# Kernel tuning notes

Measured on AMD Instinct MI355X. Metric: run time of the kernel, lower is better.

The kernel has to match this reference:

```python
import jax, jax.numpy as jnp
import numpy as np

NUM_GROUPS = 8
EPS = 1e-6


def group_norm(x, scale, bias):
    # x: [b, c, h, w]
    b, c, h, w = x.shape
    g = NUM_GROUPS
    xg = x.reshape(b, g, c // g, h, w)
    mean = jnp.mean(xg, axis=(2, 3, 4), keepdims=True)
    var = jnp.var(xg, axis=(2, 3, 4), keepdims=True)
    xg = (xg - mean) * jax.lax.rsqrt(var + EPS)
    xn = xg.reshape(b, c, h, w)
    return xn * scale[None, :, None, None] + bias[None, :, None, None]


def conv1x1(x, w, b):
    # 1x1 conv == channel-mixing matmul. x: [b,c,h,w], w: [co,ci], b: [co]
    return jnp.einsum('oc,bchw->bohw', w, x) + b[None, :, None, None]


def setup_inputs() -> dict:
    key = jax.random.key(0)
    ks = jax.random.split(key, 11)
    b, c, h, w = 8, 256, 64, 64
    s = 1.0 / np.sqrt(c)
    return {
        'x': jax.random.normal(ks[0], (b, c, h, w), dtype=jnp.float32),
        'gn_scale': jnp.ones((c,), dtype=jnp.float32),
        'gn_bias': jnp.zeros((c,), dtype=jnp.float32),
        'wq': jax.random.normal(ks[1], (c, c), dtype=jnp.float32) * s,
        'bq': jax.random.normal(ks[2], (c,), dtype=jnp.float32) * 0.01,
        'wk': jax.random.normal(ks[3], (c, c), dtype=jnp.float32) * s,
        'bk': jax.random.normal(ks[4], (c,), dtype=jnp.float32) * 0.01,
        'wv': jax.random.normal(ks[5], (c, c), dtype=jnp.float32) * s,
        'bv': jax.random.normal(ks[6], (c,), dtype=jnp.float32) * 0.01,
        'wo': jax.random.normal(ks[7], (c, c), dtype=jnp.float32) * s,
        'bo': jax.random.normal(ks[8], (c,), dtype=jnp.float32) * 0.01,
    }


def reference(x, gn_scale, gn_bias, wq, bq, wk, bk, wv, bv, wo, bo):
    b, c, h, w = x.shape
    hn = group_norm(x, gn_scale, gn_bias)
    q = conv1x1(hn, wq, bq).reshape(b, c, h * w)  # [b,c,n]
    k = conv1x1(hn, wk, bk).reshape(b, c, h * w)
    v = conv1x1(hn, wv, bv).reshape(b, c, h * w)
    scale = jnp.asarray(c, x.dtype) ** -0.5
    attn = jnp.einsum('bci,bcj->bij', q, k) * scale  # [b,n,n]
    attn = jax.nn.softmax(attn, axis=2)
    out = jnp.einsum('bcj,bij->bci', v, attn)  # [b,c,n]
    out = out.reshape(b, c, h, w)
    return x + conv1x1(out, wo, bo)
```

## Files before the change

kernel.cpp:

```cpp
#include <hip/hip_runtime.h>

typedef __bf16 bf16;
typedef __bf16 bf16x8 __attribute__((ext_vector_type(8)));
typedef float  f32x4  __attribute__((ext_vector_type(4)));

#define NSP 4096
#define NCH 256
#define NB  8

static __device__ __forceinline__ void glds16(const bf16* g, bf16* l) {
  __builtin_amdgcn_global_load_lds(
      (const __attribute__((address_space(1))) unsigned int*)g,
      (__attribute__((address_space(3))) unsigned int*)l, 16, 0, 0);
}

__global__ __launch_bounds__(256) void k_wconv(
    const float* __restrict__ wq, const float* __restrict__ wk,
    const float* __restrict__ wv, const float* __restrict__ wo,
    bf16* __restrict__ wbf) {
  int g = blockIdx.x * 256 + threadIdx.x;
  int m = g >> 16, idx = g & 65535;
  const float* src = (m == 0) ? wq : (m == 1) ? wk : (m == 2) ? wv : wo;
  float sc = (m == 0) ? 0.0625f : 1.0f;
  wbf[g] = (bf16)(src[idx] * sc);
}

__global__ __launch_bounds__(256) void k_gnstats1(const float* __restrict__ x,
                                                  float2* __restrict__ part) {
  int blk = blockIdx.x;
  int bg = blk >> 3, seg = blk & 7;
  const float4* p = (const float4*)(x + (size_t)bg * 131072 + seg * 16384);
  float s = 0.f, s2 = 0.f;
  for (int i = threadIdx.x; i < 4096; i += 256) {
    float4 v = p[i];
    s  += v.x + v.y + v.z + v.w;
    s2 += v.x*v.x + v.y*v.y + v.z*v.z + v.w*v.w;
  }
  for (int off = 1; off < 64; off <<= 1) {
    s  += __shfl_xor(s, off);
    s2 += __shfl_xor(s2, off);
  }
  __shared__ float a1[4], a2[4];
  int w = threadIdx.x >> 6, lane = threadIdx.x & 63;
  if (lane == 0) { a1[w] = s; a2[w] = s2; }
  __syncthreads();
  if (threadIdx.x == 0)
    part[blk] = make_float2(a1[0]+a1[1]+a1[2]+a1[3], a2[0]+a2[1]+a2[2]+a2[3]);
}

__global__ __launch_bounds__(64) void k_gnstats2(const float2* __restrict__ part,
                                                 float* __restrict__ stats) {
  int bg = threadIdx.x;
  float s = 0.f, s2 = 0.f;
  #pragma unroll
  for (int k = 0; k < 8; ++k) {
    float2 v = part[bg * 8 + k];
    s += v.x; s2 += v.y;
  }
  float mean = s * (1.f / 131072.f);
  float var  = s2 * (1.f / 131072.f) - mean * mean;
  stats[bg * 2]     = mean;
  stats[bg * 2 + 1] = rsqrtf(var + 1e-6f);
}

__global__ __launch_bounds__(256) void k_gnapply(const float* __restrict__ x,
    const float* __restrict__ stats, const float* __restrict__ gsc,
    const float* __restrict__ gbi, bf16* __restrict__ hnT) {
  __shared__ float T[64][65];
  int blk = blockIdx.x;
  int b = blk >> 8, ct = (blk >> 6) & 3, it = blk & 63;
  int tid = threadIdx.x;
  #pragma unroll 4
  for (int p = 0; p < 16; ++p) {
    int cc = p * 4 + (tid >> 6), ii = tid & 63;
    int c = ct * 64 + cc;
    float mean = stats[(b * 8 + (c >> 5)) * 2];
    float rstd = stats[(b * 8 + (c >> 5)) * 2 + 1];
    float v = x[((size_t)b * NCH + c) * NSP + it * 64 + ii];
    T[cc][ii] = (v - mean) * rstd * gsc[c] + gbi[c];
  }
  __syncthreads();
  #pragma unroll 4
  for (int p = 0; p < 16; ++p) {
    int ii = p * 4 + (tid >> 6), cc = tid & 63;
    hnT[((size_t)b * NSP + it * 64 + ii) * NCH + ct * 64 + cc] = (bf16)T[cc][ii];
  }
}

__global__ __launch_bounds__(256, 4) void k_qkv(const bf16* __restrict__ hnT,
    const bf16* __restrict__ wbf, const float* __restrict__ bq,
    const float* __restrict__ bk, const float* __restrict__ bv,
    bf16* __restrict__ qT, bf16* __restrict__ kS, bf16* __restrict__ vS) {
  const int pass = blockIdx.x >> 9;
  const int rem  = blockIdx.x & 511;
  const int b  = rem >> 6;
  const int i0 = (rem & 63) * 64;
  const int tid = threadIdx.x, w = tid >> 6, lane = tid & 63;
  const int li = lane & 15, qd = lane >> 4;
  const bf16* W = wbf + (size_t)pass * 65536;

  if (pass == 2) {
    f32x4 acc[16];
    #pragma unroll
    for (int t = 0; t < 16; ++t) acc[t] = (f32x4){0.f, 0.f, 0.f, 0.f};
    for (int kc = 0; kc < 8; ++kc) {
      bf16x8 hb = *(const bf16x8*)(hnT + ((size_t)b * NSP + i0 + w * 16 + li) * NCH + kc * 32 + qd * 8);
      #pragma unroll
      for (int ct = 0; ct < 16; ++ct) {
        bf16x8 wf = *(const bf16x8*)(W + (size_t)(ct * 16 + li) * NCH + kc * 32 + qd * 8);
        acc[ct] = __builtin_amdgcn_mfma_f32_16x16x32_bf16(hb, wf, acc[ct], 0, 0, 0);
      }
    }
    int jloc = w * 16 + qd * 4;
    size_t base = (size_t)b * 1048576 + (size_t)((i0 + jloc) >> 5) * 8192;
    int j32 = jloc & 31;
    int g  = (j32 >> 2) & 3;
    int hi = j32 >> 4;
    #pragma unroll
    for (int ct = 0; ct < 16; ++ct) {
      int co = ct * 16 + li;
      float bb = bv[co];
      int pg = g ^ ((co >> 1) & 3);
      union { bf16 h[4]; uint2 u; } pk;
      #pragma unroll
      for (int r = 0; r < 4; ++r) pk.h[r] = (bf16)(acc[ct][r] + bb);
      *(uint2*)(vS + base + (size_t)(co * 4 + pg) * 8 + hi * 4) = pk.u;
    }
    return;
  }

  f32x4 acc[16];
  #pragma unroll
  for (int t = 0; t < 16; ++t) acc[t] = (f32x4){0.f, 0.f, 0.f, 0.f};
  for (int kc = 0; kc < 8; ++kc) {
    bf16x8 hb[4];
    #pragma unroll
    for (int nt = 0; nt < 4; ++nt)
      hb[nt] = *(const bf16x8*)(hnT + ((size_t)b * NSP + i0 + nt * 16 + li) * NCH + kc * 32 + qd * 8);
    #pragma unroll
    for (int mt = 0; mt < 4; ++mt) {
      bf16x8 wf = *(const bf16x8*)(W + (size_t)(w * 64 + mt * 16 + li) * NCH + kc * 32 + qd * 8);
      #pragma unroll
      for (int nt = 0; nt < 4; ++nt)
        acc[mt * 4 + nt] = __builtin_amdgcn_mfma_f32_16x16x32_bf16(wf, hb[nt], acc[mt * 4 + nt], 0, 0, 0);
    }
  }

  if (pass == 0) {
    bf16* out = qT + ((size_t)b * NSP + i0) * NCH;
    #pragma unroll
    for (int mt = 0; mt < 4; ++mt) {
      float bb[4];
      #pragma unroll
      for (int r = 0; r < 4; ++r) bb[r] = bq[w * 64 + mt * 16 + qd * 4 + r] * 0.0625f;
      #pragma unroll
      for (int nt = 0; nt < 4; ++nt) {
        union { bf16 h[4]; uint2 u; } pk;
        #pragma unroll
        for (int r = 0; r < 4; ++r) pk.h[r] = (bf16)(acc[mt * 4 + nt][r] + bb[r]);
        *(uint2*)(out + (size_t)(nt * 16 + li) * NCH + w * 64 + mt * 16 + qd * 4) = pk.u;
      }
    }
  } else {
    #pragma unroll
    for (int mt = 0; mt < 4; ++mt) {
      float bb[4];
      #pragma unroll
      for (int r = 0; r < 4; ++r) bb[r] = bk[w * 64 + mt * 16 + qd * 4 + r];
      int cb = w * 8 + mt * 2 + (qd >> 1);
      #pragma unroll
      for (int nt = 0; nt < 4; ++nt) {
        int jloc = nt * 16 + li;
        size_t base = (size_t)b * 1048576 + (size_t)((i0 + jloc) >> 5) * 8192;
        int r32 = jloc & 31;
        union { bf16 h[4]; uint2 u; } pk;
        #pragma unroll
        for (int r = 0; r < 4; ++r) pk.h[r] = (bf16)(acc[mt * 4 + nt][r] + bb[r]);
        *(uint2*)(kS + base + r32 * 256 + (cb ^ (r32 & 7)) * 8 + (qd & 1) * 4) = pk.u;
      }
    }
  }
}

__global__ __launch_bounds__(256, 2) void k_attn(const bf16* __restrict__ qT,
    const bf16* __restrict__ kS, const bf16* __restrict__ vS,
    bf16* __restrict__ Op0, bf16* __restrict__ Op1, float* __restrict__ Lp) {
  __shared__ bf16 Kb[2][8192];
  __shared__ bf16 Vt[8192];

  const int bjs = blockIdx.x & 15;
  const int itb = blockIdx.x >> 4;
  const int b = bjs >> 1, js = bjs & 1;
  const int i0 = itb * 128;
  const int tid = threadIdx.x, w = tid >> 6, lane = tid & 63;
  const int li = lane & 15, qd = lane >> 4;

  const bf16* kS_b = kS + (size_t)b * 1048576 + (size_t)js * 524288;
  const bf16* vS_b = vS + (size_t)b * 1048576 + (size_t)js * 524288;

  bf16x8 qf[2][8];
  #pragma unroll
  for (int it = 0; it < 2; ++it) {
    const bf16* qp = qT + ((size_t)b * NSP + i0 + w * 32 + it * 16 + li) * NCH + qd * 8;
    #pragma unroll
    for (int kc = 0; kc < 8; ++kc) qf[it][kc] = *(const bf16x8*)(qp + kc * 32);
  }

  f32x4 Oa[2][16];
  #pragma unroll
  for (int it = 0; it < 2; ++it)
    #pragma unroll
    for (int t = 0; t < 16; ++t) Oa[it][t] = (f32x4){0.f, 0.f, 0.f, 0.f};
  float lacc[2] = {0.f, 0.f};

  int4 Rv[4];
  #pragma unroll
  for (int p = 0; p < 4; ++p)
    glds16(kS_b + (size_t)(w * 256 + p * 64 + lane) * 8, &Kb[0][(w * 256 + p * 64) * 8]);
  #pragma unroll
  for (int p = 0; p < 4; ++p)
    Rv[p] = *(const int4*)(vS_b + (size_t)(p * 256 + tid) * 8);

  const int pgv = qd ^ ((li >> 1) & 3);

  for (int jc = 0; jc < 64; ++jc) {
    const int cur = jc & 1;
    __syncthreads();
    #pragma unroll
    for (int p = 0; p < 4; ++p)
      *(int4*)(&Vt[(size_t)(p * 256 + tid) * 8]) = Rv[p];
    __syncthreads();

    {
      const int jn = (jc < 63) ? jc + 1 : 63;
      const bf16* kt = kS_b + (size_t)jn * 8192;
      const bf16* vt = vS_b + (size_t)jn * 8192;
      #pragma unroll
      for (int p = 0; p < 4; ++p)
        glds16(kt + (size_t)(w * 256 + p * 64 + lane) * 8, &Kb[cur ^ 1][(w * 256 + p * 64) * 8]);
      #pragma unroll
      for (int p = 0; p < 4; ++p)
        Rv[p] = *(const int4*)(vt + (size_t)(p * 256 + tid) * 8);
    }

    const bf16* Kc = Kb[cur];
    f32x4 S[2][2];
    S[0][0] = (f32x4){0.f,0.f,0.f,0.f}; S[0][1] = (f32x4){0.f,0.f,0.f,0.f};
    S[1][0] = (f32x4){0.f,0.f,0.f,0.f}; S[1][1] = (f32x4){0.f,0.f,0.f,0.f};
    #pragma unroll
    for (int jt = 0; jt < 2; ++jt) {
      #pragma unroll
      for (int kc = 0; kc < 8; ++kc) {
        int pb = (kc * 4 + qd) ^ (li & 7);
        bf16x8 kf = *(const bf16x8*)(Kc + (jt * 16 + li) * 256 + pb * 8);
        S[0][jt] = __builtin_amdgcn_mfma_f32_16x16x32_bf16(kf, qf[0][kc], S[0][jt], 0, 0, 0);
        S[1][jt] = __builtin_amdgcn_mfma_f32_16x16x32_bf16(kf, qf[1][kc], S[1][jt], 0, 0, 0);
      }
    }

    bf16x8 pf[2];
    #pragma unroll
    for (int it = 0; it < 2; ++it)
      #pragma unroll
      for (int jt = 0; jt < 2; ++jt)
        #pragma unroll
        for (int r = 0; r < 4; ++r) {
          float e = __expf(S[it][jt][r] - 8.f);
          lacc[it] += e;
          pf[it][jt * 4 + r] = (bf16)e;
        }

    #pragma unroll
    for (int ct = 0; ct < 16; ++ct) {
      bf16x8 vf = *(const bf16x8*)(&Vt[(size_t)(ct * 16 + li) * 32 + pgv * 8]);
      Oa[0][ct] = __builtin_amdgcn_mfma_f32_16x16x32_bf16(vf, pf[0], Oa[0][ct], 0, 0, 0);
      Oa[1][ct] = __builtin_amdgcn_mfma_f32_16x16x32_bf16(vf, pf[1], Oa[1][ct], 0, 0, 0);
    }
  }

  float lfull[2], linv[2];
  #pragma unroll
  for (int it = 0; it < 2; ++it) {
    float v = lacc[it];
    v += __shfl_xor(v, 16);
    v += __shfl_xor(v, 32);
    lfull[it] = v;
    linv[it] = 1.f / v;
  }

  bf16* Op = js ? Op1 : Op0;
  #pragma unroll
  for (int it = 0; it < 2; ++it) {
    bf16* op = Op + ((size_t)b * NSP + i0 + w * 32 + it * 16 + li) * NCH;
    #pragma unroll
    for (int ct = 0; ct < 16; ++ct) {
      union { bf16 h[4]; uint2 u; } pk;
      pk.h[0] = (bf16)(Oa[it][ct][0] * linv[it]);
      pk.h[1] = (bf16)(Oa[it][ct][1] * linv[it]);
      pk.h[2] = (bf16)(Oa[it][ct][2] * linv[it]);
      pk.h[3] = (bf16)(Oa[it][ct][3] * linv[it]);
      *(uint2*)(op + ct * 16 + qd * 4) = pk.u;
    }
  }
  if (qd == 0) {
    float* lp = Lp + js * 32768 + b * 4096 + i0 + w * 32;
    #pragma unroll
    for (int it = 0; it < 2; ++it) lp[it * 16 + li] = lfull[it];
  }
}

__global__ __launch_bounds__(256, 4) void k_out(const bf16* __restrict__ Op0,
    const bf16* __restrict__ Op1, const float* __restrict__ Lp,
    const bf16* __restrict__ wo, const float* __restrict__ bo,
    const float* __restrict__ x, float* __restrict__ out) {
  const int b  = blockIdx.x >> 7;
  const int i0 = ((blockIdx.x >> 1) & 63) * 64;
  const int ch = blockIdx.x & 1;
  const int tid = threadIdx.x, w = tid >> 6, lane = tid & 63;
  const int li = lane & 15, qd = lane >> 4;
  const int cb0 = ch * 128 + w * 32;

  float w0[4], w1[4];
  #pragma unroll
  for (int nt = 0; nt < 4; ++nt) {
    int i = b * 4096 + i0 + nt * 16 + li;
    float l0 = Lp[i], l1 = Lp[32768 + i];
    float inv = 1.f / (l0 + l1);
    w0[nt] = l0 * inv; w1[nt] = l1 * inv;
  }

  f32x4 acc[8];
  #pragma unroll
  for (int t = 0; t < 8; ++t) acc[t] = (f32x4){0.f, 0.f, 0.f, 0.f};
  for (int kc = 0; kc < 8; ++kc) {
    bf16x8 ab[4];
    #pragma unroll
    for (int nt = 0; nt < 4; ++nt) {
      size_t off = ((size_t)b * NSP + i0 + nt * 16 + li) * NCH + kc * 32 + qd * 8;
      bf16x8 a0 = *(const bf16x8*)(Op0 + off);
      bf16x8 a1 = *(const bf16x8*)(Op1 + off);
      #pragma unroll
      for (int e = 0; e < 8; ++e)
        ab[nt][e] = (bf16)(w0[nt] * (float)a0[e] + w1[nt] * (float)a1[e]);
    }
    #pragma unroll
    for (int mt = 0; mt < 2; ++mt) {
      bf16x8 wf = *(const bf16x8*)(wo + (size_t)(cb0 + mt * 16 + li) * NCH + kc * 32 + qd * 8);
      #pragma unroll
      for (int nt = 0; nt < 4; ++nt)
        acc[mt * 4 + nt] = __builtin_amdgcn_mfma_f32_16x16x32_bf16(wf, ab[nt], acc[mt * 4 + nt], 0, 0, 0);
    }
  }
  #pragma unroll
  for (int mt = 0; mt < 2; ++mt) {
    #pragma unroll
    for (int r = 0; r < 4; ++r) {
      int co = cb0 + mt * 16 + qd * 4 + r;
      float bb = bo[co];
      #pragma unroll
      for (int nt = 0; nt < 4; ++nt) {
        size_t idx = ((size_t)b * NCH + co) * NSP + i0 + nt * 16 + li;
        out[idx] = acc[mt * 4 + nt][r] + bb + x[idx];
      }
    }
  }
}

extern "C" void kernel_launch(void* const* d_in, const int* in_sizes, int n_in,
                              void* d_out, int out_size, void* d_ws, size_t ws_size,
                              hipStream_t stream) {
  (void)in_sizes; (void)n_in; (void)out_size; (void)ws_size;
  const float* x   = (const float*)d_in[0];
  const float* gsc = (const float*)d_in[1];
  const float* gbi = (const float*)d_in[2];
  const float* wq  = (const float*)d_in[3];
  const float* bq  = (const float*)d_in[4];
  const float* wk  = (const float*)d_in[5];
  const float* bk  = (const float*)d_in[6];
  const float* wv  = (const float*)d_in[7];
  const float* bv  = (const float*)d_in[8];
  const float* wo  = (const float*)d_in[9];
  const float* bo  = (const float*)d_in[10];

  char* ws = (char*)d_ws;
  const size_t MB16 = 16777216u;
  bf16*   wbf   = (bf16*)(ws);
  float*  stats = (float*)(ws + 524288);
  float2* part  = (float2*)(ws + 528384);
  float*  Lp    = (float*)(ws + 655360);
  bf16*   hnT   = (bf16*)(ws + (1u << 20));
  bf16*   qT    = (bf16*)(ws + (1u << 20) + 1 * MB16);
  bf16*   kS    = (bf16*)(ws + (1u << 20) + 2 * MB16);
  bf16*   vS    = (bf16*)(ws + (1u << 20) + 3 * MB16);
  bf16*   Op1   = (bf16*)(ws + (1u << 20) + 4 * MB16);
  bf16*   Op0   = hnT;
  float*  out   = (float*)d_out;

  k_wconv   <<<1024, 256, 0, stream>>>(wq, wk, wv, wo, wbf);
  k_gnstats1<<< 512, 256, 0, stream>>>(x, part);
  k_gnstats2<<<   1,  64, 0, stream>>>(part, stats);
  k_gnapply <<<2048, 256, 0, stream>>>(x, stats, gsc, gbi, hnT);
  k_qkv     <<<1536, 256, 0, stream>>>(hnT, wbf, bq, bk, bv, qT, kS, vS);
  k_attn    <<< 512, 256, 0, stream>>>(qT, kS, vS, Op0, Op1, Lp);
  k_out     <<<1024, 256, 0, stream>>>(Op0, Op1, Lp, wbf + 3ull * 65536, bo, x, out);
}
```

Baseline: 456.4 us.

## Merge prep kernels, fuse QKV passes via LDS, stream V directly in attention

Merges the weight-conversion and group-norm statistics kernels into a single launch. The QKV kernel now stages each hidden tile in swizzled LDS once and computes Q, K and V from it in one block, instead of using three separate block sets that each reread hnT. The attention kernel drops the V LDS staging and its extra barrier, changes the vS layout so each lane can load its V fragments straight from global memory interleaved with the QK MFMAs, and stops issuing the redundant final K prefetch. In exchange the attention loop takes on global-load latency and higher register pressure, and the QKV grid shrinks to 512 blocks, which reduces parallelism.

```diff
diff --git a/kernel.cpp b/kernel.cpp
--- a/kernel.cpp
+++ b/kernel.cpp
@@ -14,38 +14,37 @@
       (__attribute__((address_space(3))) unsigned int*)l, 16, 0, 0);
 }
 
-__global__ __launch_bounds__(256) void k_wconv(
+__global__ __launch_bounds__(256) void k_prep(const float* __restrict__ x,
     const float* __restrict__ wq, const float* __restrict__ wk,
     const float* __restrict__ wv, const float* __restrict__ wo,
-    bf16* __restrict__ wbf) {
-  int g = blockIdx.x * 256 + threadIdx.x;
-  int m = g >> 16, idx = g & 65535;
-  const float* src = (m == 0) ? wq : (m == 1) ? wk : (m == 2) ? wv : wo;
-  float sc = (m == 0) ? 0.0625f : 1.0f;
-  wbf[g] = (bf16)(src[idx] * sc);
-}
-
-__global__ __launch_bounds__(256) void k_gnstats1(const float* __restrict__ x,
-                                                  float2* __restrict__ part) {
-  int blk = blockIdx.x;
-  int bg = blk >> 3, seg = blk & 7;
-  const float4* p = (const float4*)(x + (size_t)bg * 131072 + seg * 16384);
-  float s = 0.f, s2 = 0.f;
-  for (int i = threadIdx.x; i < 4096; i += 256) {
-    float4 v = p[i];
-    s  += v.x + v.y + v.z + v.w;
-    s2 += v.x*v.x + v.y*v.y + v.z*v.z + v.w*v.w;
-  }
-  for (int off = 1; off < 64; off <<= 1) {
-    s  += __shfl_xor(s, off);
-    s2 += __shfl_xor(s2, off);
-  }
-  __shared__ float a1[4], a2[4];
-  int w = threadIdx.x >> 6, lane = threadIdx.x & 63;
-  if (lane == 0) { a1[w] = s; a2[w] = s2; }
-  __syncthreads();
-  if (threadIdx.x == 0)
-    part[blk] = make_float2(a1[0]+a1[1]+a1[2]+a1[3], a2[0]+a2[1]+a2[2]+a2[3]);
+    bf16* __restrict__ wbf, float2* __restrict__ part) {
+  if (blockIdx.x < 512) {
+    int blk = blockIdx.x;
+    int bg = blk >> 3, seg = blk & 7;
+    const float4* p = (const float4*)(x + (size_t)bg * 131072 + seg * 16384);
+    float s = 0.f, s2 = 0.f;
+    for (int i = threadIdx.x; i < 4096; i += 256) {
+      float4 v = p[i];
+      s  += v.x + v.y + v.z + v.w;
+      s2 += v.x*v.x + v.y*v.y + v.z*v.z + v.w*v.w;
+    }
+    for (int off = 1; off < 64; off <<= 1) {
+      s  += __shfl_xor(s, off);
+      s2 += __shfl_xor(s2, off);
+    }
+    __shared__ float a1[4], a2[4];
+    int w = threadIdx.x >> 6, lane = threadIdx.x & 63;
+    if (lane == 0) { a1[w] = s; a2[w] = s2; }
+    __syncthreads();
+    if (threadIdx.x == 0)
+      part[blk] = make_float2(a1[0]+a1[1]+a1[2]+a1[3], a2[0]+a2[1]+a2[2]+a2[3]);
+  } else {
+    int g = (blockIdx.x - 512) * 256 + threadIdx.x;
+    int m = g >> 16, idx = g & 65535;
+    const float* src = (m == 0) ? wq : (m == 1) ? wk : (m == 2) ? wv : wo;
+    float sc = (m == 0) ? 0.0625f : 1.0f;
+    wbf[g] = (bf16)(src[idx] * sc);
+  }
 }
 
 __global__ __launch_bounds__(64) void k_gnstats2(const float2* __restrict__ part,
@@ -91,20 +90,83 @@
     const bf16* __restrict__ wbf, const float* __restrict__ bq,
     const float* __restrict__ bk, const float* __restrict__ bv,
     bf16* __restrict__ qT, bf16* __restrict__ kS, bf16* __restrict__ vS) {
-  const int pass = blockIdx.x >> 9;
-  const int rem  = blockIdx.x & 511;
-  const int b  = rem >> 6;
-  const int i0 = (rem & 63) * 64;
+  __shared__ bf16 hnS[64 * 256];
+  const int b  = blockIdx.x >> 6;
+  const int i0 = (blockIdx.x & 63) * 64;
   const int tid = threadIdx.x, w = tid >> 6, lane = tid & 63;
   const int li = lane & 15, qd = lane >> 4;
-  const bf16* W = wbf + (size_t)pass * 65536;
-
-  if (pass == 2) {
+
+  #pragma unroll
+  for (int p = 0; p < 8; ++p) {
+    int idx = p * 256 + tid;
+    int i = idx >> 5, g = idx & 31;
+    bf16x8 v = *(const bf16x8*)(hnT + ((size_t)b * NSP + i0 + i) * NCH + g * 8);
+    *(bf16x8*)(&hnS[i * 256 + (g ^ (i & 7)) * 8]) = v;
+  }
+  __syncthreads();
+
+  #pragma unroll 1
+  for (int pass = 0; pass < 2; ++pass) {
+    const bf16* W = wbf + (size_t)pass * 65536;
     f32x4 acc[16];
     #pragma unroll
     for (int t = 0; t < 16; ++t) acc[t] = (f32x4){0.f, 0.f, 0.f, 0.f};
     for (int kc = 0; kc < 8; ++kc) {
-      bf16x8 hb = *(const bf16x8*)(hnT + ((size_t)b * NSP + i0 + w * 16 + li) * NCH + kc * 32 + qd * 8);
+      bf16x8 hb[4];
+      #pragma unroll
+      for (int nt = 0; nt < 4; ++nt)
+        hb[nt] = *(const bf16x8*)(&hnS[(nt * 16 + li) * 256 + ((kc * 4 + qd) ^ (li & 7)) * 8]);
+      #pragma unroll
+      for (int mt = 0; mt < 4; ++mt) {
+        bf16x8 wf = *(const bf16x8*)(W + (size_t)(w * 64 + mt * 16 + li) * NCH + kc * 32 + qd * 8);
+        #pragma unroll
+        for (int nt = 0; nt < 4; ++nt)
+          acc[mt * 4 + nt] = __builtin_amdgcn_mfma_f32_16x16x32_bf16(wf, hb[nt], acc[mt * 4 + nt], 0, 0, 0);
+      }
+    }
+    if (pass == 0) {
+      bf16* out = qT + ((size_t)b * NSP + i0) * NCH;
+      #pragma unroll
+      for (int mt = 0; mt < 4; ++mt) {
+        float bb[4];
+        #pragma unroll
+        for (int r = 0; r < 4; ++r) bb[r] = bq[w * 64 + mt * 16 + qd * 4 + r] * 0.0625f;
+        #pragma unroll
+        for (int nt = 0; nt < 4; ++nt) {
+          union { bf16 h[4]; uint2 u; } pk;
+          #pragma unroll
+          for (int r = 0; r < 4; ++r) pk.h[r] = (bf16)(acc[mt * 4 + nt][r] + bb[r]);
+          *(uint2*)(out + (size_t)(nt * 16 + li) * NCH + w * 64 + mt * 16 + qd * 4) = pk.u;
+        }
+      }
+    } else {
+      #pragma unroll
+      for (int mt = 0; mt < 4; ++mt) {
+        float bb[4];
+        #pragma unroll
+        for (int r = 0; r < 4; ++r) bb[r] = bk[w * 64 + mt * 16 + qd * 4 + r];
+        int cb = w * 8 + mt * 2 + (qd >> 1);
+        #pragma unroll
+        for (int nt = 0; nt < 4; ++nt) {
+          int jloc = nt * 16 + li;
+          size_t base = (size_t)b * 1048576 + (size_t)((i0 + jloc) >> 5) * 8192;
+          int r32 = jloc & 31;
+          union { bf16 h[4]; uint2 u; } pk;
+          #pragma unroll
+          for (int r = 0; r < 4; ++r) pk.h[r] = (bf16)(acc[mt * 4 + nt][r] + bb[r]);
+          *(uint2*)(kS + base + r32 * 256 + (cb ^ (r32 & 7)) * 8 + (qd & 1) * 4) = pk.u;
+        }
+      }
+    }
+  }
+
+  {
+    const bf16* W = wbf + 2ull * 65536;
+    f32x4 acc[16];
+    #pragma unroll
+    for (int t = 0; t < 16; ++t) acc[t] = (f32x4){0.f, 0.f, 0.f, 0.f};
+    for (int kc = 0; kc < 8; ++kc) {
+      bf16x8 hb = *(const bf16x8*)(&hnS[(w * 16 + li) * 256 + ((kc * 4 + qd) ^ (li & 7)) * 8]);
       #pragma unroll
       for (int ct = 0; ct < 16; ++ct) {
         bf16x8 wf = *(const bf16x8*)(W + (size_t)(ct * 16 + li) * NCH + kc * 32 + qd * 8);
@@ -113,71 +175,14 @@
     }
     int jloc = w * 16 + qd * 4;
     size_t base = (size_t)b * 1048576 + (size_t)((i0 + jloc) >> 5) * 8192;
-    int j32 = jloc & 31;
-    int g  = (j32 >> 2) & 3;
-    int hi = j32 >> 4;
     #pragma unroll
     for (int ct = 0; ct < 16; ++ct) {
       int co = ct * 16 + li;
       float bb = bv[co];
-      int pg = g ^ ((co >> 1) & 3);
       union { bf16 h[4]; uint2 u; } pk;
       #pragma unroll
       for (int r = 0; r < 4; ++r) pk.h[r] = (bf16)(acc[ct][r] + bb);
-      *(uint2*)(vS + base + (size_t)(co * 4 + pg) * 8 + hi * 4) = pk.u;
-    }
-    return;
-  }
-
-  f32x4 acc[16];
-  #pragma unroll
-  for (int t = 0; t < 16; ++t) acc[t] = (f32x4){0.f, 0.f, 0.f, 0.f};
-  for (int kc = 0; kc < 8; ++kc) {
-    bf16x8 hb[4];
-    #pragma unroll
-    for (int nt = 0; nt < 4; ++nt)
-      hb[nt] = *(const bf16x8*)(hnT + ((size_t)b * NSP + i0 + nt * 16 + li) * NCH + kc * 32 + qd * 8);
-    #pragma unroll
-    for (int mt = 0; mt < 4; ++mt) {
-      bf16x8 wf = *(const bf16x8*)(W + (size_t)(w * 64 + mt * 16 + li) * NCH + kc * 32 + qd * 8);
-      #pragma unroll
-      for (int nt = 0; nt < 4; ++nt)
-        acc[mt * 4 + nt] = __builtin_amdgcn_mfma_f32_16x16x32_bf16(wf, hb[nt], acc[mt * 4 + nt], 0, 0, 0);
-    }
-  }
-
-  if (pass == 0) {
-    bf16* out = qT + ((size_t)b * NSP + i0) * NCH;
-    #pragma unroll
-    for (int mt = 0; mt < 4; ++mt) {
-      float bb[4];
-      #pragma unroll
-      for (int r = 0; r < 4; ++r) bb[r] = bq[w * 64 + mt * 16 + qd * 4 + r] * 0.0625f;
-      #pragma unroll
-      for (int nt = 0; nt < 4; ++nt) {
-        union { bf16 h[4]; uint2 u; } pk;
-        #pragma unroll
-        for (int r = 0; r < 4; ++r) pk.h[r] = (bf16)(acc[mt * 4 + nt][r] + bb[r]);
-        *(uint2*)(out + (size_t)(nt * 16 + li) * NCH + w * 64 + mt * 16 + qd * 4) = pk.u;
-      }
-    }
-  } else {
-    #pragma unroll
-    for (int mt = 0; mt < 4; ++mt) {
-      float bb[4];
-      #pragma unroll
-      for (int r = 0; r < 4; ++r) bb[r] = bk[w * 64 + mt * 16 + qd * 4 + r];
-      int cb = w * 8 + mt * 2 + (qd >> 1);
-      #pragma unroll
-      for (int nt = 0; nt < 4; ++nt) {
-        int jloc = nt * 16 + li;
-        size_t base = (size_t)b * 1048576 + (size_t)((i0 + jloc) >> 5) * 8192;
-        int r32 = jloc & 31;
-        union { bf16 h[4]; uint2 u; } pk;
-        #pragma unroll
-        for (int r = 0; r < 4; ++r) pk.h[r] = (bf16)(acc[mt * 4 + nt][r] + bb[r]);
-        *(uint2*)(kS + base + r32 * 256 + (cb ^ (r32 & 7)) * 8 + (qd & 1) * 4) = pk.u;
-      }
+      *(uint2*)(vS + base + (size_t)co * 32 + qd * 8 + (w & 1) * 4) = pk.u;
     }
   }
 }
@@ -186,7 +191,6 @@
     const bf16* __restrict__ kS, const bf16* __restrict__ vS,
     bf16* __restrict__ Op0, bf16* __restrict__ Op1, float* __restrict__ Lp) {
   __shared__ bf16 Kb[2][8192];
-  __shared__ bf16 Vt[8192];
 
   const int bjs = blockIdx.x & 15;
   const int itb = blockIdx.x >> 4;
@@ -196,7 +200,8 @@
   const int li = lane & 15, qd = lane >> 4;
 
   const bf16* kS_b = kS + (size_t)b * 1048576 + (size_t)js * 524288;
-  const bf16* vS_b = vS + (size_t)b * 1048576 + (size_t)js * 524288;
+  const bf16* vS_b = vS + (size_t)b * 1048576 + (size_t)js * 524288
+                   + li * 32 + qd * 8;
 
   bf16x8 qf[2][8];
   #pragma unroll
@@ -213,50 +218,47 @@
     for (int t = 0; t < 16; ++t) Oa[it][t] = (f32x4){0.f, 0.f, 0.f, 0.f};
   float lacc[2] = {0.f, 0.f};
 
-  int4 Rv[4];
   #pragma unroll
   for (int p = 0; p < 4; ++p)
     glds16(kS_b + (size_t)(w * 256 + p * 64 + lane) * 8, &Kb[0][(w * 256 + p * 64) * 8]);
-  #pragma unroll
-  for (int p = 0; p < 4; ++p)
-    Rv[p] = *(const int4*)(vS_b + (size_t)(p * 256 + tid) * 8);
-
-  const int pgv = qd ^ ((li >> 1) & 3);
 
   for (int jc = 0; jc < 64; ++jc) {
     const int cur = jc & 1;
     __syncthreads();
-    #pragma unroll
-    for (int p = 0; p < 4; ++p)
-      *(int4*)(&Vt[(size_t)(p * 256 + tid) * 8]) = Rv[p];
-    __syncthreads();
-
-    {
-      const int jn = (jc < 63) ? jc + 1 : 63;
-      const bf16* kt = kS_b + (size_t)jn * 8192;
-      const bf16* vt = vS_b + (size_t)jn * 8192;
+    if (jc < 63) {
+      const bf16* kt = kS_b + (size_t)(jc + 1) * 8192;
       #pragma unroll
       for (int p = 0; p < 4; ++p)
         glds16(kt + (size_t)(w * 256 + p * 64 + lane) * 8, &Kb[cur ^ 1][(w * 256 + p * 64) * 8]);
-      #pragma unroll
-      for (int p = 0; p < 4; ++p)
-        Rv[p] = *(const int4*)(vt + (size_t)(p * 256 + tid) * 8);
-    }
+    }
+    const bf16* vt = vS_b + (size_t)jc * 8192;
+
+    bf16x8 vf0[4], vf1[4], vf2[4], vf3[4];
+    #pragma unroll
+    for (int u = 0; u < 4; ++u) vf0[u] = *(const bf16x8*)(vt + u * 512);
 
     const bf16* Kc = Kb[cur];
     f32x4 S[2][2];
     S[0][0] = (f32x4){0.f,0.f,0.f,0.f}; S[0][1] = (f32x4){0.f,0.f,0.f,0.f};
     S[1][0] = (f32x4){0.f,0.f,0.f,0.f}; S[1][1] = (f32x4){0.f,0.f,0.f,0.f};
     #pragma unroll
-    for (int jt = 0; jt < 2; ++jt) {
-      #pragma unroll
-      for (int kc = 0; kc < 8; ++kc) {
-        int pb = (kc * 4 + qd) ^ (li & 7);
-        bf16x8 kf = *(const bf16x8*)(Kc + (jt * 16 + li) * 256 + pb * 8);
-        S[0][jt] = __builtin_amdgcn_mfma_f32_16x16x32_bf16(kf, qf[0][kc], S[0][jt], 0, 0, 0);
-        S[1][jt] = __builtin_amdgcn_mfma_f32_16x16x32_bf16(kf, qf[1][kc], S[1][jt], 0, 0, 0);
-      }
-    }
+    for (int kc = 0; kc < 8; ++kc) {
+      int pb = (kc * 4 + qd) ^ (li & 7);
+      bf16x8 kf = *(const bf16x8*)(Kc + li * 256 + pb * 8);
+      S[0][0] = __builtin_amdgcn_mfma_f32_16x16x32_bf16(kf, qf[0][kc], S[0][0], 0, 0, 0);
+      S[1][0] = __builtin_amdgcn_mfma_f32_16x16x32_bf16(kf, qf[1][kc], S[1][0], 0, 0, 0);
+    }
+    #pragma unroll
+    for (int u = 0; u < 4; ++u) vf1[u] = *(const bf16x8*)(vt + (4 + u) * 512);
+    #pragma unroll
+    for (int kc = 0; kc < 8; ++kc) {
+      int pb = (kc * 4 + qd) ^ (li & 7);
+      bf16x8 kf = *(const bf16x8*)(Kc + (16 + li) * 256 + pb * 8);
+      S[0][1] = __builtin_amdgcn_mfma_f32_16x16x32_bf16(kf, qf[0][kc], S[0][1], 0, 0, 0);
+      S[1][1] = __builtin_amdgcn_mfma_f32_16x16x32_bf16(kf, qf[1][kc], S[1][1], 0, 0, 0);
+    }
+    #pragma unroll
+    for (int u = 0; u < 4; ++u) vf2[u] = *(const bf16x8*)(vt + (8 + u) * 512);
 
     bf16x8 pf[2];
     #pragma unroll
@@ -269,12 +271,28 @@
           lacc[it] += e;
           pf[it][jt * 4 + r] = (bf16)e;
         }
-
-    #pragma unroll
-    for (int ct = 0; ct < 16; ++ct) {
-      bf16x8 vf = *(const bf16x8*)(&Vt[(size_t)(ct * 16 + li) * 32 + pgv * 8]);
-      Oa[0][ct] = __builtin_amdgcn_mfma_f32_16x16x32_bf16(vf, pf[0], Oa[0][ct], 0, 0, 0);
-      Oa[1][ct] = __builtin_amdgcn_mfma_f32_16x16x32_bf16(vf, pf[1], Oa[1][ct], 0, 0, 0);
+    #pragma unroll
+    for (int u = 0; u < 4; ++u) vf3[u] = *(const bf16x8*)(vt + (12 + u) * 512);
+
+    #pragma unroll
+    for (int u = 0; u < 4; ++u) {
+      Oa[0][u] = __builtin_amdgcn_mfma_f32_16x16x32_bf16(vf0[u], pf[0], Oa[0][u], 0, 0, 0);
+      Oa[1][u] = __builtin_amdgcn_mfma_f32_16x16x32_bf16(vf0[u], pf[1], Oa[1][u], 0, 0, 0);
+    }
+    #pragma unroll
+    for (int u = 0; u < 4; ++u) {
+      Oa[0][4 + u] = __builtin_amdgcn_mfma_f32_16x16x32_bf16(vf1[u], pf[0], Oa[0][4 + u], 0, 0, 0);
+      Oa[1][4 + u] = __builtin_amdgcn_mfma_f32_16x16x32_bf16(vf1[u], pf[1], Oa[1][4 + u], 0, 0, 0);
+    }
+    #pragma unroll
+    for (int u = 0; u < 4; ++u) {
+      Oa[0][8 + u] = __builtin_amdgcn_mfma_f32_16x16x32_bf16(vf2[u], pf[0], Oa[0][8 + u], 0, 0, 0);
+      Oa[1][8 + u] = __builtin_amdgcn_mfma_f32_16x16x32_bf16(vf2[u], pf[1], Oa[1][8 + u], 0, 0, 0);
+    }
+    #pragma unroll
+    for (int u = 0; u < 4; ++u) {
+      Oa[0][12 + u] = __builtin_amdgcn_mfma_f32_16x16x32_bf16(vf3[u], pf[0], Oa[0][12 + u], 0, 0, 0);
+      Oa[1][12 + u] = __builtin_amdgcn_mfma_f32_16x16x32_bf16(vf3[u], pf[1], Oa[1][12 + u], 0, 0, 0);
     }
   }
 
@@ -396,11 +414,10 @@
   bf16*   Op0   = hnT;
   float*  out   = (float*)d_out;
 
-  k_wconv   <<<1024, 256, 0, stream>>>(wq, wk, wv, wo, wbf);
-  k_gnstats1<<< 512, 256, 0, stream>>>(x, part);
+  k_prep    <<<1536, 256, 0, stream>>>(x, wq, wk, wv, wo, wbf, part);
   k_gnstats2<<<   1,  64, 0, stream>>>(part, stats);
   k_gnapply <<<2048, 256, 0, stream>>>(x, stats, gsc, gbi, hnT);
-  k_qkv     <<<1536, 256, 0, stream>>>(hnT, wbf, bq, bk, bv, qT, kS, vS);
+  k_qkv     <<< 512, 256, 0, stream>>>(hnT, wbf, bq, bk, bv, qT, kS, vS);
   k_attn    <<< 512, 256, 0, stream>>>(qT, kS, vS, Op0, Op1, Lp);
   k_out     <<<1024, 256, 0, stream>>>(Op0, Op1, Lp, wbf + 3ull * 65536, bo, x, out);
 }
```

Result: slower. 551.0 us (+20.7%).

## Fuse groupnorm apply into QKV projection, merge prep kernels, async-load V in attention

Applied to the files above, without the earlier changes.

Merges the weight-conversion and groupnorm-statistics kernels into one launch. Fuses the groupnorm apply and transpose into the QKV kernel, which builds a swizzled bf16 tile in LDS and computes Q, K and V from it, removing the hnT round trip through global memory. The attention kernel now double-buffers V in LDS using direct global-to-LDS loads instead of staging through registers, which drops a barrier per iteration. The QKV grid shrinks to 512 blocks with more LDS and serial passes per block, so occupancy and parallelism go down.

```diff
diff --git a/kernel.cpp b/kernel.cpp
--- a/kernel.cpp
+++ b/kernel.cpp
@@ -14,38 +14,37 @@
       (__attribute__((address_space(3))) unsigned int*)l, 16, 0, 0);
 }
 
-__global__ __launch_bounds__(256) void k_wconv(
+__global__ __launch_bounds__(256) void k_prep(const float* __restrict__ x,
     const float* __restrict__ wq, const float* __restrict__ wk,
     const float* __restrict__ wv, const float* __restrict__ wo,
-    bf16* __restrict__ wbf) {
-  int g = blockIdx.x * 256 + threadIdx.x;
-  int m = g >> 16, idx = g & 65535;
-  const float* src = (m == 0) ? wq : (m == 1) ? wk : (m == 2) ? wv : wo;
-  float sc = (m == 0) ? 0.0625f : 1.0f;
-  wbf[g] = (bf16)(src[idx] * sc);
-}
-
-__global__ __launch_bounds__(256) void k_gnstats1(const float* __restrict__ x,
-                                                  float2* __restrict__ part) {
-  int blk = blockIdx.x;
-  int bg = blk >> 3, seg = blk & 7;
-  const float4* p = (const float4*)(x + (size_t)bg * 131072 + seg * 16384);
-  float s = 0.f, s2 = 0.f;
-  for (int i = threadIdx.x; i < 4096; i += 256) {
-    float4 v = p[i];
-    s  += v.x + v.y + v.z + v.w;
-    s2 += v.x*v.x + v.y*v.y + v.z*v.z + v.w*v.w;
-  }
-  for (int off = 1; off < 64; off <<= 1) {
-    s  += __shfl_xor(s, off);
-    s2 += __shfl_xor(s2, off);
-  }
-  __shared__ float a1[4], a2[4];
-  int w = threadIdx.x >> 6, lane = threadIdx.x & 63;
-  if (lane == 0) { a1[w] = s; a2[w] = s2; }
-  __syncthreads();
-  if (threadIdx.x == 0)
-    part[blk] = make_float2(a1[0]+a1[1]+a1[2]+a1[3], a2[0]+a2[1]+a2[2]+a2[3]);
+    bf16* __restrict__ wbf, float2* __restrict__ part) {
+  if (blockIdx.x < 512) {
+    int blk = blockIdx.x;
+    int bg = blk >> 3, seg = blk & 7;
+    const float4* p = (const float4*)(x + (size_t)bg * 131072 + seg * 16384);
+    float s = 0.f, s2 = 0.f;
+    for (int i = threadIdx.x; i < 4096; i += 256) {
+      float4 v = p[i];
+      s  += v.x + v.y + v.z + v.w;
+      s2 += v.x*v.x + v.y*v.y + v.z*v.z + v.w*v.w;
+    }
+    for (int off = 1; off < 64; off <<= 1) {
+      s  += __shfl_xor(s, off);
+      s2 += __shfl_xor(s2, off);
+    }
+    __shared__ float a1[4], a2[4];
+    int w = threadIdx.x >> 6, lane = threadIdx.x & 63;
+    if (lane == 0) { a1[w] = s; a2[w] = s2; }
+    __syncthreads();
+    if (threadIdx.x == 0)
+      part[blk] = make_float2(a1[0]+a1[1]+a1[2]+a1[3], a2[0]+a2[1]+a2[2]+a2[3]);
+  } else {
+    int g = (blockIdx.x - 512) * 256 + threadIdx.x;
+    int m = g >> 16, idx = g & 65535;
+    const float* src = (m == 0) ? wq : (m == 1) ? wk : (m == 2) ? wv : wo;
+    float sc = (m == 0) ? 0.0625f : 1.0f;
+    wbf[g] = (bf16)(src[idx] * sc);
+  }
 }
 
 __global__ __launch_bounds__(64) void k_gnstats2(const float2* __restrict__ part,
@@ -63,48 +62,107 @@
   stats[bg * 2 + 1] = rsqrtf(var + 1e-6f);
 }
 
-__global__ __launch_bounds__(256) void k_gnapply(const float* __restrict__ x,
+__global__ __launch_bounds__(256, 3) void k_qkv(const float* __restrict__ x,
     const float* __restrict__ stats, const float* __restrict__ gsc,
-    const float* __restrict__ gbi, bf16* __restrict__ hnT) {
+    const float* __restrict__ gbi, const bf16* __restrict__ wbf,
+    const float* __restrict__ bq, const float* __restrict__ bk,
+    const float* __restrict__ bv,
+    bf16* __restrict__ qT, bf16* __restrict__ kS, bf16* __restrict__ vS) {
   __shared__ float T[64][65];
-  int blk = blockIdx.x;
-  int b = blk >> 8, ct = (blk >> 6) & 3, it = blk & 63;
-  int tid = threadIdx.x;
-  #pragma unroll 4
-  for (int p = 0; p < 16; ++p) {
-    int cc = p * 4 + (tid >> 6), ii = tid & 63;
-    int c = ct * 64 + cc;
-    float mean = stats[(b * 8 + (c >> 5)) * 2];
-    float rstd = stats[(b * 8 + (c >> 5)) * 2 + 1];
-    float v = x[((size_t)b * NCH + c) * NSP + it * 64 + ii];
-    T[cc][ii] = (v - mean) * rstd * gsc[c] + gbi[c];
-  }
-  __syncthreads();
-  #pragma unroll 4
-  for (int p = 0; p < 16; ++p) {
-    int ii = p * 4 + (tid >> 6), cc = tid & 63;
-    hnT[((size_t)b * NSP + it * 64 + ii) * NCH + ct * 64 + cc] = (bf16)T[cc][ii];
-  }
-}
-
-__global__ __launch_bounds__(256, 4) void k_qkv(const bf16* __restrict__ hnT,
-    const bf16* __restrict__ wbf, const float* __restrict__ bq,
-    const float* __restrict__ bk, const float* __restrict__ bv,
-    bf16* __restrict__ qT, bf16* __restrict__ kS, bf16* __restrict__ vS) {
-  const int pass = blockIdx.x >> 9;
-  const int rem  = blockIdx.x & 511;
-  const int b  = rem >> 6;
-  const int i0 = (rem & 63) * 64;
+  __shared__ bf16 hnS[64 * 256];
+  const int b  = blockIdx.x >> 6;
+  const int i0 = (blockIdx.x & 63) * 64;
   const int tid = threadIdx.x, w = tid >> 6, lane = tid & 63;
   const int li = lane & 15, qd = lane >> 4;
-  const bf16* W = wbf + (size_t)pass * 65536;
-
-  if (pass == 2) {
+
+  for (int ct = 0; ct < 4; ++ct) {
+    if (ct) __syncthreads();
+    #pragma unroll 4
+    for (int p = 0; p < 16; ++p) {
+      int cc = p * 4 + (tid >> 6), ii = tid & 63;
+      int c = ct * 64 + cc;
+      float mean = stats[(b * 8 + (c >> 5)) * 2];
+      float rstd = stats[(b * 8 + (c >> 5)) * 2 + 1];
+      float v = x[((size_t)b * NCH + c) * NSP + i0 + ii];
+      T[cc][ii] = (v - mean) * rstd * gsc[c] + gbi[c];
+    }
+    __syncthreads();
+    #pragma unroll
+    for (int h = 0; h < 2; ++h) {
+      int oid = h * 256 + tid;
+      int g8 = oid & 7;
+      int i  = oid >> 3;
+      bf16x8 pk;
+      #pragma unroll
+      for (int e = 0; e < 8; ++e) pk[e] = (bf16)T[g8 * 8 + e][i];
+      int g = ct * 8 + g8;
+      *(bf16x8*)(&hnS[i * 256 + (g ^ (i & 7)) * 8]) = pk;
+    }
+  }
+  __syncthreads();
+
+  #pragma unroll 1
+  for (int pass = 0; pass < 2; ++pass) {
+    const bf16* W = wbf + (size_t)pass * 65536;
     f32x4 acc[16];
     #pragma unroll
     for (int t = 0; t < 16; ++t) acc[t] = (f32x4){0.f, 0.f, 0.f, 0.f};
     for (int kc = 0; kc < 8; ++kc) {
-      bf16x8 hb = *(const bf16x8*)(hnT + ((size_t)b * NSP + i0 + w * 16 + li) * NCH + kc * 32 + qd * 8);
+      bf16x8 hb[4];
+      #pragma unroll
+      for (int nt = 0; nt < 4; ++nt)
+        hb[nt] = *(const bf16x8*)(&hnS[(nt * 16 + li) * 256 + ((kc * 4 + qd) ^ (li & 7)) * 8]);
+      #pragma unroll
+      for (int mt = 0; mt < 4; ++mt) {
+        bf16x8 wf = *(const bf16x8*)(W + (size_t)(w * 64 + mt * 16 + li) * NCH + kc * 32 + qd * 8);
+        #pragma unroll
+        for (int nt = 0; nt < 4; ++nt)
+          acc[mt * 4 + nt] = __builtin_amdgcn_mfma_f32_16x16x32_bf16(wf, hb[nt], acc[mt * 4 + nt], 0, 0, 0);
+      }
+    }
+    if (pass == 0) {
+      bf16* out = qT + ((size_t)b * NSP + i0) * NCH;
+      #pragma unroll
+      for (int mt = 0; mt < 4; ++mt) {
+        float bb[4];
+        #pragma unroll
+        for (int r = 0; r < 4; ++r) bb[r] = bq[w * 64 + mt * 16 + qd * 4 + r] * 0.0625f;
+        #pragma unroll
+        for (int nt = 0; nt < 4; ++nt) {
+          union { bf16 h[4]; uint2 u; } pk;
+          #pragma unroll
+          for (int r = 0; r < 4; ++r) pk.h[r] = (bf16)(acc[mt * 4 + nt][r] + bb[r]);
+          *(uint2*)(out + (size_t)(nt * 16 + li) * NCH + w * 64 + mt * 16 + qd * 4) = pk.u;
+        }
+      }
+    } else {
+      #pragma unroll
+      for (int mt = 0; mt < 4; ++mt) {
+        float bb[4];
+        #pragma unroll
+        for (int r = 0; r < 4; ++r) bb[r] = bk[w * 64 + mt * 16 + qd * 4 + r];
+        int cb = w * 8 + mt * 2 + (qd >> 1);
+        #pragma unroll
+        for (int nt = 0; nt < 4; ++nt) {
+          int jloc = nt * 16 + li;
+          size_t base = (size_t)b * 1048576 + (size_t)((i0 + jloc) >> 5) * 8192;
+          int r32 = jloc & 31;
+          union { bf16 h[4]; uint2 u; } pk;
+          #pragma unroll
+          for (int r = 0; r < 4; ++r) pk.h[r] = (bf16)(acc[mt * 4 + nt][r] + bb[r]);
+          *(uint2*)(kS + base + r32 * 256 + (cb ^ (r32 & 7)) * 8 + (qd & 1) * 4) = pk.u;
+        }
+      }
+    }
+  }
+
+  {
+    const bf16* W = wbf + 2ull * 65536;
+    f32x4 acc[16];
+    #pragma unroll
+    for (int t = 0; t < 16; ++t) acc[t] = (f32x4){0.f, 0.f, 0.f, 0.f};
+    for (int kc = 0; kc < 8; ++kc) {
+      bf16x8 hb = *(const bf16x8*)(&hnS[(w * 16 + li) * 256 + ((kc * 4 + qd) ^ (li & 7)) * 8]);
       #pragma unroll
       for (int ct = 0; ct < 16; ++ct) {
         bf16x8 wf = *(const bf16x8*)(W + (size_t)(ct * 16 + li) * NCH + kc * 32 + qd * 8);
@@ -113,71 +171,16 @@
     }
     int jloc = w * 16 + qd * 4;
     size_t base = (size_t)b * 1048576 + (size_t)((i0 + jloc) >> 5) * 8192;
-    int j32 = jloc & 31;
-    int g  = (j32 >> 2) & 3;
-    int hi = j32 >> 4;
+    int hi = (jloc >> 4) & 1;
     #pragma unroll
     for (int ct = 0; ct < 16; ++ct) {
       int co = ct * 16 + li;
       float bb = bv[co];
-      int pg = g ^ ((co >> 1) & 3);
+      int pg = qd ^ ((co >> 1) & 3);
       union { bf16 h[4]; uint2 u; } pk;
       #pragma unroll
       for (int r = 0; r < 4; ++r) pk.h[r] = (bf16)(acc[ct][r] + bb);
       *(uint2*)(vS + base + (size_t)(co * 4 + pg) * 8 + hi * 4) = pk.u;
-    }
-    return;
-  }
-
-  f32x4 acc[16];
-  #pragma unroll
-  for (int t = 0; t < 16; ++t) acc[t] = (f32x4){0.f, 0.f, 0.f, 0.f};
-  for (int kc = 0; kc < 8; ++kc) {
-    bf16x8 hb[4];
-    #pragma unroll
-    for (int nt = 0; nt < 4; ++nt)
-      hb[nt] = *(const bf16x8*)(hnT + ((size_t)b * NSP + i0 + nt * 16 + li) * NCH + kc * 32 + qd * 8);
-    #pragma unroll
-    for (int mt = 0; mt < 4; ++mt) {
-      bf16x8 wf = *(const bf16x8*)(W + (size_t)(w * 64 + mt * 16 + li) * NCH + kc * 32 + qd * 8);
-      #pragma unroll
-      for (int nt = 0; nt < 4; ++nt)
-        acc[mt * 4 + nt] = __builtin_amdgcn_mfma_f32_16x16x32_bf16(wf, hb[nt], acc[mt * 4 + nt], 0, 0, 0);
-    }
-  }
-
-  if (pass == 0) {
-    bf16* out = qT + ((size_t)b * NSP + i0) * NCH;
-    #pragma unroll
-    for (int mt = 0; mt < 4; ++mt) {
-      float bb[4];
-      #pragma unroll
-      for (int r = 0; r < 4; ++r) bb[r] = bq[w * 64 + mt * 16 + qd * 4 + r] * 0.0625f;
-      #pragma unroll
-      for (int nt = 0; nt < 4; ++nt) {
-        union { bf16 h[4]; uint2 u; } pk;
-        #pragma unroll
-        for (int r = 0; r < 4; ++r) pk.h[r] = (bf16)(acc[mt * 4 + nt][r] + bb[r]);
-        *(uint2*)(out + (size_t)(nt * 16 + li) * NCH + w * 64 + mt * 16 + qd * 4) = pk.u;
-      }
-    }
-  } else {
-    #pragma unroll
-    for (int mt = 0; mt < 4; ++mt) {
-      float bb[4];
-      #pragma unroll
-      for (int r = 0; r < 4; ++r) bb[r] = bk[w * 64 + mt * 16 + qd * 4 + r];
-      int cb = w * 8 + mt * 2 + (qd >> 1);
-      #pragma unroll
-      for (int nt = 0; nt < 4; ++nt) {
-        int jloc = nt * 16 + li;
-        size_t base = (size_t)b * 1048576 + (size_t)((i0 + jloc) >> 5) * 8192;
-        int r32 = jloc & 31;
-        union { bf16 h[4]; uint2 u; } pk;
-        #pragma unroll
-        for (int r = 0; r < 4; ++r) pk.h[r] = (bf16)(acc[mt * 4 + nt][r] + bb[r]);
-        *(uint2*)(kS + base + r32 * 256 + (cb ^ (r32 & 7)) * 8 + (qd & 1) * 4) = pk.u;
-      }
     }
   }
 }
@@ -186,7 +189,7 @@
     const bf16* __restrict__ kS, const bf16* __restrict__ vS,
     bf16* __restrict__ Op0, bf16* __restrict__ Op1, float* __restrict__ Lp) {
   __shared__ bf16 Kb[2][8192];
-  __shared__ bf16 Vt[8192];
+  __shared__ bf16 Vb[2][8192];
 
   const int bjs = blockIdx.x & 15;
   const int itb = blockIdx.x >> 4;
@@ -213,34 +216,27 @@
     for (int t = 0; t < 16; ++t) Oa[it][t] = (f32x4){0.f, 0.f, 0.f, 0.f};
   float lacc[2] = {0.f, 0.f};
 
-  int4 Rv[4];
   #pragma unroll
   for (int p = 0; p < 4; ++p)
     glds16(kS_b + (size_t)(w * 256 + p * 64 + lane) * 8, &Kb[0][(w * 256 + p * 64) * 8]);
   #pragma unroll
   for (int p = 0; p < 4; ++p)
-    Rv[p] = *(const int4*)(vS_b + (size_t)(p * 256 + tid) * 8);
+    glds16(vS_b + (size_t)(w * 256 + p * 64 + lane) * 8, &Vb[0][(w * 256 + p * 64) * 8]);
 
   const int pgv = qd ^ ((li >> 1) & 3);
 
   for (int jc = 0; jc < 64; ++jc) {
     const int cur = jc & 1;
     __syncthreads();
-    #pragma unroll
-    for (int p = 0; p < 4; ++p)
-      *(int4*)(&Vt[(size_t)(p * 256 + tid) * 8]) = Rv[p];
-    __syncthreads();
-
-    {
-      const int jn = (jc < 63) ? jc + 1 : 63;
-      const bf16* kt = kS_b + (size_t)jn * 8192;
-      const bf16* vt = vS_b + (size_t)jn * 8192;
+    if (jc < 63) {
+      const bf16* kt = kS_b + (size_t)(jc + 1) * 8192;
+      const bf16* vt = vS_b + (size_t)(jc + 1) * 8192;
       #pragma unroll
       for (int p = 0; p < 4; ++p)
         glds16(kt + (size_t)(w * 256 + p * 64 + lane) * 8, &Kb[cur ^ 1][(w * 256 + p * 64) * 8]);
       #pragma unroll
       for (int p = 0; p < 4; ++p)
-        Rv[p] = *(const int4*)(vt + (size_t)(p * 256 + tid) * 8);
+        glds16(vt + (size_t)(w * 256 + p * 64 + lane) * 8, &Vb[cur ^ 1][(w * 256 + p * 64) * 8]);
     }
 
     const bf16* Kc = Kb[cur];
@@ -270,9 +266,10 @@
           pf[it][jt * 4 + r] = (bf16)e;
         }
 
+    const bf16* Vc = Vb[cur];
     #pragma unroll
     for (int ct = 0; ct < 16; ++ct) {
-      bf16x8 vf = *(const bf16x8*)(&Vt[(size_t)(ct * 16 + li) * 32 + pgv * 8]);
+      bf16x8 vf = *(const bf16x8*)(Vc + (size_t)(ct * 16 + li) * 32 + pgv * 8);
       Oa[0][ct] = __builtin_amdgcn_mfma_f32_16x16x32_bf16(vf, pf[0], Oa[0][ct], 0, 0, 0);
       Oa[1][ct] = __builtin_amdgcn_mfma_f32_16x16x32_bf16(vf, pf[1], Oa[1][ct], 0, 0, 0);
     }
@@ -388,19 +385,16 @@
   float*  stats = (float*)(ws + 524288);
   float2* part  = (float2*)(ws + 528384);
   float*  Lp    = (float*)(ws + 655360);
-  bf16*   hnT   = (bf16*)(ws + (1u << 20));
+  bf16*   Op0   = (bf16*)(ws + (1u << 20));
   bf16*   qT    = (bf16*)(ws + (1u << 20) + 1 * MB16);
   bf16*   kS    = (bf16*)(ws + (1u << 20) + 2 * MB16);
   bf16*   vS    = (bf16*)(ws + (1u << 20) + 3 * MB16);
   bf16*   Op1   = (bf16*)(ws + (1u << 20) + 4 * MB16);
-  bf16*   Op0   = hnT;
   float*  out   = (float*)d_out;
 
-  k_wconv   <<<1024, 256, 0, stream>>>(wq, wk, wv, wo, wbf);
-  k_gnstats1<<< 512, 256, 0, stream>>>(x, part);
+  k_prep    <<<1536, 256, 0, stream>>>(x, wq, wk, wv, wo, wbf, part);
   k_gnstats2<<<   1,  64, 0, stream>>>(part, stats);
-  k_gnapply <<<2048, 256, 0, stream>>>(x, stats, gsc, gbi, hnT);
-  k_qkv     <<<1536, 256, 0, stream>>>(hnT, wbf, bq, bk, bv, qT, kS, vS);
+  k_qkv     <<< 512, 256, 0, stream>>>(x, stats, gsc, gbi, wbf, bq, bk, bv, qT, kS, vS);
   k_attn    <<< 512, 256, 0, stream>>>(qT, kS, vS, Op0, Op1, Lp);
   k_out     <<<1024, 256, 0, stream>>>(Op0, Op1, Lp, wbf + 3ull * 65536, bo, x, out);
 }
```

Measured after the change: 370.2 us. 18.9% less time.
